# Performance work log

Measured on AMD Instinct MI355X. Metric: run time of the kernel, lower is better.

The kernel has to match this reference:

```python
import jax, jax.numpy as jnp
import numpy as np

H = 32          # total heads
K = 8           # active heads per token
D = 128         # head_dim = embed_dim // active_heads
E = 1024        # embed_dim
S = 1024        # seq_len
MAX_SEQ = 8192
BASE = 10000.0
SCALE = D ** -0.5
LB_W = 0.01
ENT_W = 0.01


def _rope(v, cos, sin):
    # v: (T, D); cos/sin: (T, D)
    v1, v2 = v[:, : D // 2], v[:, D // 2:]
    rot = jnp.concatenate([-v2, v1], axis=-1)
    return v * cos + rot * sin


def setup_inputs() -> dict:
    key = jax.random.key(0)
    ks = jax.random.split(key, 6)
    x = jax.random.normal(ks[0], (1, S, E), jnp.float32)
    Wq = jax.random.normal(ks[1], (E, H * D), jnp.float32) * 0.02
    Wk = jax.random.normal(ks[2], (E, H * D), jnp.float32) * 0.02
    Wv = jax.random.normal(ks[3], (E, H * D), jnp.float32) * 0.02
    Wr = jax.random.normal(ks[4], (E, H), jnp.float32) * 0.02
    Wo = jax.random.normal(ks[5], (K * D, E), jnp.float32) * 0.02
    head_counts = jnp.zeros((1, H), jnp.int32)
    return {"x": x, "Wq": Wq, "Wk": Wk, "Wv": Wv, "Wr": Wr, "Wo": Wo,
            "head_counts": head_counts}


def reference(x, Wq, Wk, Wv, Wr, Wo, head_counts):
    # ---- routing (eval mode: no gumbel noise) ----
    logits = x @ Wr                                   # (1, S, H)
    soft_probs = jax.nn.softmax(logits, axis=-1)
    top_logits, head_idx = jax.lax.top_k(logits, K)   # (1, S, K)
    head_w = jax.nn.softmax(top_logits, axis=-1)      # (1, S, K)

    # ---- aux loss ----
    primary = head_idx[..., 0]                        # (1, S)
    one_hot_p = jax.nn.one_hot(primary, H, dtype=jnp.float32)
    f = one_hot_p.mean(axis=1)                        # (1, H)
    p = soft_probs.mean(axis=1)                       # (1, H)
    balance = H * (f * p).sum(axis=-1).mean()
    entropy = -(soft_probs * jnp.log(soft_probs + 1e-8)).sum(axis=-1)
    entropy_loss = -entropy.mean()
    z_loss = (jax.nn.logsumexp(logits, axis=-1) ** 2).mean() * 0.01
    aux_loss = LB_W * balance + ENT_W * entropy_loss + z_loss

    # ---- projections + per-token gather of selected heads ----
    q_all = (x @ Wq).reshape(1, S, H, D)
    k_all = (x @ Wk).reshape(1, S, H, D)
    v_all = (x @ Wv).reshape(1, S, H, D)
    gidx = head_idx[..., None]                        # (1, S, K, 1)
    q = jnp.take_along_axis(q_all, gidx, axis=2)[0].reshape(S * K, D)
    k = jnp.take_along_axis(k_all, gidx, axis=2)[0].reshape(S * K, D)
    v = jnp.take_along_axis(v_all, gidx, axis=2)[0].reshape(S * K, D)

    heads_flat = head_idx[0].reshape(S * K)           # (T,)

    # rank of each dispatched token within its head (exclusive prefix count)
    oh = jax.nn.one_hot(heads_flat, H, dtype=jnp.int32)   # (T, H)
    excl = jnp.cumsum(oh, axis=0) - oh
    rank = jnp.take_along_axis(excl, heads_flat[:, None], axis=1)[:, 0]
    positions = rank + head_counts[0, heads_flat]
    positions = jnp.clip(positions, 0, MAX_SEQ - 1)

    # ---- per-head RoPE with per-head position counters ----
    inv_freq = 1.0 / (BASE ** (jnp.arange(0, D, 2, dtype=jnp.float32) / D))
    freqs = positions.astype(jnp.float32)[:, None] * inv_freq[None, :]
    emb = jnp.concatenate([freqs, freqs], axis=-1)    # (T, D)
    cos, sin = jnp.cos(emb), jnp.sin(emb)
    q = _rope(q, cos, sin)
    k = _rope(k, cos, sin)

    # ---- block-diagonal-causal attention (same head, earlier dispatch order) ----
    idx = jnp.arange(S * K)
    mask = (heads_flat[:, None] == heads_flat[None, :]) & (idx[None, :] <= idx[:, None])
    scores = (q @ k.T) * SCALE                        # (T, T)
    scores = jnp.where(mask, scores, jnp.float32(-1e30))
    attn = jax.nn.softmax(scores, axis=-1)
    out = attn @ v                                    # (T, D)

    # ---- combine with routing weights + output projection ----
    out = out.reshape(S, K, D) * head_w[0][..., None]
    out = out.reshape(S, K * D) @ Wo                  # (S, E)
    output = out[None]                                # (1, S, E)

    updated_counts = head_counts + oh.sum(axis=0)[None]
    return output, updated_counts, aux_loss
```

## Files before the change

### kernel.cpp

```cpp
#include <hip/hip_runtime.h>
#include <math.h>

#define S 1024
#define E 1024
#define H 32
#define KSEL 8
#define D 128
#define HD 4096
#define SK 8192
#define MAXL 1024
#define CAP 9216
#define ATTN_SCALE 0.08838834764831845f
#define SSTR 36
#define PSTR 40

#define NROUTER 256
#define NCONV 832

typedef _Float16 half8 __attribute__((ext_vector_type(8)));
typedef _Float16 half4 __attribute__((ext_vector_type(4)));
typedef float floatx4 __attribute__((ext_vector_type(4)));
typedef float floatx16 __attribute__((ext_vector_type(16)));
typedef float f4 __attribute__((ext_vector_type(4)));

#define GLOAD_LDS16(gsrc, ldst) \
    __builtin_amdgcn_global_load_lds( \
        (const __attribute__((address_space(1))) void*)(gsrc), \
        (__attribute__((address_space(3))) void*)(ldst), 16, 0, 0)

__global__ __launch_bounds__(256) void router_conv_kernel(
    const float* __restrict__ x, const float* __restrict__ Wr,
    int* __restrict__ head_idx, float* __restrict__ head_w,
    float* __restrict__ pbuf, float* __restrict__ entz,
    _Float16* __restrict__ xh,
    const float* __restrict__ Wq, const float* __restrict__ Wk,
    const float* __restrict__ Wv, const float* __restrict__ Wo,
    _Float16* __restrict__ Wqkt, _Float16* __restrict__ Wot)
{
    int bid = blockIdx.x, tid = threadIdx.x;
    if (bid >= NROUTER) {
        __shared__ _Float16 tl[128 * 128];
        int cb = bid - NROUTER;
        int z, rem;
        if (cb < 768) { z = cb >> 8; rem = cb & 255; }
        else          { z = 3;       rem = cb - 768; }
        const float* W = (z == 0) ? Wq : (z == 1) ? Wk : (z == 2) ? Wv : Wo;
        _Float16* T = (z < 3) ? (Wqkt + (size_t)z * HD * E) : Wot;
        int C = (z < 3) ? HD : 1024;
        int nc = C >> 7;
        int c0 = (rem % nc) * 128;
        int r0 = (rem / nc) * 128;
        #pragma unroll
        for (int p = 0; p < 16; ++p) {
            int idx = p * 256 + tid;
            int rr = idx >> 5, cg = (idx & 31) * 4;
            f4 v = *(const f4*)&W[(size_t)(r0 + rr) * C + c0 + cg];
            half4 o;
            o.x = (_Float16)v.x; o.y = (_Float16)v.y;
            o.z = (_Float16)v.z; o.w = (_Float16)v.w;
            int sc = cg ^ (((rr >> 3) & 7) << 2);
            *(half4*)&tl[rr * 128 + sc] = o;
        }
        __syncthreads();
        #pragma unroll
        for (int p = 0; p < 8; ++p) {
            int chunk = p * 256 + tid;
            int cc = chunk >> 4, ch = chunk & 15;
            int cidx = cc ^ ((ch & 7) << 2);
            half8 o;
            #pragma unroll
            for (int j = 0; j < 8; ++j)
                o[j] = tl[(ch * 8 + j) * 128 + cidx];
            *(half8*)&T[(size_t)(c0 + cc) * 1024 + r0 + ch * 8] = o;
        }
        return;
    }
    int s = bid * 4 + (tid >> 6);
    int lane = tid & 63;
    int h = lane & 31, half = lane >> 5;
    const float* xr = x + (size_t)s * E + half * 512;
    const float* wr = Wr + (size_t)(half * 512) * H + h;
    float a0 = 0.f, a1 = 0.f, a2 = 0.f, a3 = 0.f;
    #pragma unroll 4
    for (int e = 0; e < 512; e += 4) {
        a0 += xr[e]     * wr[e * H];
        a1 += xr[e + 1] * wr[(e + 1) * H];
        a2 += xr[e + 2] * wr[(e + 2) * H];
        a3 += xr[e + 3] * wr[(e + 3) * H];
    }
    float acc = (a0 + a1) + (a2 + a3);
    acc += __shfl_xor(acc, 32, 64);
    float logit = acc;
    float m = logit;
    #pragma unroll
    for (int off = 16; off; off >>= 1) m = fmaxf(m, __shfl_xor(m, off, 64));
    float ex = expf(logit - m);
    float Z = ex;
    #pragma unroll
    for (int off = 16; off; off >>= 1) Z += __shfl_xor(Z, off, 64);
    float p = ex / Z;
    float es = p * logf(p + 1e-8f);
    #pragma unroll
    for (int off = 16; off; off >>= 1) es += __shfl_xor(es, off, 64);
    float lse = m + logf(Z);
    float lv = logit;
    float tv[KSEL]; int ti[KSEL];
    #pragma unroll
    for (int j = 0; j < KSEL; ++j) {
        float bv = lv; int bi = h;
        #pragma unroll
        for (int off = 16; off; off >>= 1) {
            float ov = __shfl_xor(bv, off, 64);
            int oi = __shfl_xor(bi, off, 64);
            if (ov > bv || (ov == bv && oi < bi)) { bv = ov; bi = oi; }
        }
        tv[j] = bv; ti[j] = bi;
        if (h == bi) lv = -INFINITY;
    }
    float Z2 = 0.f;
    #pragma unroll
    for (int j = 0; j < KSEL; ++j) Z2 += expf(tv[j] - tv[0]);
    if (lane < 32) pbuf[s * 32 + lane] = p;
    if (lane == 0) {
        entz[s * 2]     = es;
        entz[s * 2 + 1] = lse * lse;
        #pragma unroll
        for (int j = 0; j < KSEL; ++j) {
            head_idx[s * KSEL + j] = ti[j];
            head_w[s * KSEL + j]   = expf(tv[j] - tv[0]) / Z2;
        }
    }
    const float* xrow = x + (size_t)s * E;
    _Float16* xhrow = xh + (size_t)s * E;
    #pragma unroll
    for (int t = 0; t < 4; ++t) {
        int e = t * 256 + lane * 4;
        f4 v = *(const f4*)&xrow[e];
        half4 o;
        o.x = (_Float16)v.x; o.y = (_Float16)v.y; o.z = (_Float16)v.z; o.w = (_Float16)v.w;
        *(half4*)&xhrow[e] = o;
    }
}

__global__ __launch_bounds__(256) void scan_aux_kernel(
    const int* __restrict__ head_idx, const int* __restrict__ head_counts,
    int* __restrict__ order, int* __restrict__ hlen, float* __restrict__ out_counts,
    const float* __restrict__ pbuf, const float* __restrict__ entz,
    float* __restrict__ out_aux)
{
    int bid = blockIdx.x, tid = threadIdx.x;
    if (bid == H) {
        int hh = tid & 31, grp = tid >> 5;
        __shared__ float red[256], red2[256];
        __shared__ float psum[32];
        __shared__ int hist[32];
        if (tid < 32) hist[tid] = 0;
        float ps = 0.f;
        for (int s = grp; s < S; s += 8) ps += pbuf[s * 32 + hh];
        red[tid] = ps;
        float es = 0.f, zs = 0.f;
        for (int s = tid; s < S; s += 256) { es += entz[s * 2]; zs += entz[s * 2 + 1]; }
        red2[tid] = es;
        __syncthreads();
        if (grp == 0) {
            float v = 0.f;
            #pragma unroll
            for (int j = 0; j < 8; ++j) v += red[j * 32 + hh];
            psum[hh] = v;
        }
        __syncthreads();
        red[tid] = zs;
        for (int s = tid; s < S; s += 256)
            atomicAdd(&hist[head_idx[s * KSEL]], 1);
        __syncthreads();
        for (int stp = 128; stp; stp >>= 1) {
            if (tid < stp) { red[tid] += red[tid + stp]; red2[tid] += red2[tid + stp]; }
            __syncthreads();
        }
        if (tid == 0) {
            float bal = 0.f;
            for (int j = 0; j < H; ++j)
                bal += ((float)hist[j] / (float)S) * (psum[j] / (float)S);
            bal *= (float)H;
            float ent_loss = red2[0] / (float)S;
            float z = red[0] / (float)S * 0.01f;
            out_aux[0] = 0.01f * bal + 0.01f * ent_loss + z;
        }
        return;
    }
    int h = bid;
    int wave = tid >> 6, lane = tid & 63;
    __shared__ int wtot[4][4];
    int base = 0;
    int hc = head_counts[h];
    int v0 = head_idx[tid],       v1 = head_idx[256 + tid];
    int v2 = head_idx[512 + tid], v3 = head_idx[768 + tid];
    unsigned long long lt = (1ull << lane) - 1ull;
    for (int c0 = 0; c0 < SK; c0 += 1024) {
        int n0 = 0, n1 = 0, n2 = 0, n3 = 0;
        if (c0 + 1024 < SK) {
            n0 = head_idx[c0 + 1024 + tid]; n1 = head_idx[c0 + 1280 + tid];
            n2 = head_idx[c0 + 1536 + tid]; n3 = head_idx[c0 + 1792 + tid];
        }
        bool p0 = (v0 == h), p1 = (v1 == h), p2 = (v2 == h), p3 = (v3 == h);
        unsigned long long m0 = __ballot(p0), m1 = __ballot(p1);
        unsigned long long m2 = __ballot(p2), m3 = __ballot(p3);
        int w0 = __popcll(m0 & lt), w1 = __popcll(m1 & lt);
        int w2 = __popcll(m2 & lt), w3 = __popcll(m3 & lt);
        if (lane == 0) {
            wtot[0][wave] = __popcll(m0); wtot[1][wave] = __popcll(m1);
            wtot[2][wave] = __popcll(m2); wtot[3][wave] = __popcll(m3);
        }
        __syncthreads();
        int pw[4], T[4];
        #pragma unroll
        for (int i = 0; i < 4; ++i) {
            int pre = 0, tot = 0;
            #pragma unroll
            for (int w = 0; w < 4; ++w) {
                int tv = wtot[i][w];
                if (w < wave) pre += tv;
                tot += tv;
            }
            pw[i] = pre; T[i] = tot;
        }
        if (p0) order[h * MAXL + base + pw[0] + w0] = c0 + tid;
        if (p1) order[h * MAXL + base + T[0] + pw[1] + w1] = c0 + 256 + tid;
        if (p2) order[h * MAXL + base + T[0] + T[1] + pw[2] + w2] = c0 + 512 + tid;
        if (p3) order[h * MAXL + base + T[0] + T[1] + T[2] + pw[3] + w3] = c0 + 768 + tid;
        base += T[0] + T[1] + T[2] + T[3];
        __syncthreads();
        v0 = n0; v1 = n1; v2 = n2; v3 = n3;
    }
    if (tid == 0) {
        hlen[h] = base;
        out_counts[h] = (float)(hc + base);
    }
}

__global__ __launch_bounds__(256) void qkv_mfma(
    const _Float16* __restrict__ xh, const _Float16* __restrict__ Wt,
    const int* __restrict__ order, const int* __restrict__ hlen,
    const int* __restrict__ head_counts,
    _Float16* __restrict__ qh, _Float16* __restrict__ kh, _Float16* __restrict__ vT)
{
    int xid = blockIdx.x;
    int qkv = xid >> 5, h = xid & 31;
    int rt = blockIdx.y;
    int len = hlen[h];
    int row0 = rt * 64;
    if (row0 >= len) return;
    int hb = 0;
    for (int i = 0; i < h; ++i) hb += (hlen[i] + 31) & ~31;
    int lenp = (len + 31) & ~31;
    int tid = threadIdx.x, wave = tid >> 6, lane = tid & 63;
    int wm = wave >> 1, wn = wave & 1;
    int l32 = lane & 31, g = lane >> 5;

    __shared__ _Float16 Bs[2][128 * 64];

    int arow_g = row0 + wm * 32 + l32;
    int tok = (arow_g < len) ? (order[h * MAXL + arow_g] >> 3) : 0;
    const _Float16* aptr = xh + (size_t)tok * E;

    const _Float16* Wb = Wt + (size_t)((qkv * H + h) * D) * E;

    auto stageB = [&](int buf, int k0) {
        #pragma unroll
        for (int it = 0; it < 4; ++it) {
            int f = it * 256 + tid;
            int row = f >> 3, c = f & 7;
            int sc = c ^ (row & 7);
            const _Float16* src = Wb + (size_t)row * E + k0 + sc * 8;
            GLOAD_LDS16(src, &Bs[buf][f * 8]);
        }
    };

    floatx16 acc[2] = {};
    half8 a_cur[4], a_nxt[4];
    #pragma unroll
    for (int ks = 0; ks < 4; ++ks)
        a_cur[ks] = *(const half8*)(aptr + ks * 16 + g * 8);

    auto compute = [&](int buf, half8* a) {
        #pragma unroll
        for (int ks = 0; ks < 4; ++ks) {
            int wchunk = ks * 2 + g;
            #pragma unroll
            for (int nf = 0; nf < 2; ++nf) {
                int brow = wn * 64 + nf * 32 + l32;
                half8 bf = *(const half8*)&Bs[buf][brow * 64 + (wchunk ^ (brow & 7)) * 8];
                acc[nf] = __builtin_amdgcn_mfma_f32_32x32x16_f16(a[ks], bf, acc[nf], 0, 0, 0);
            }
        }
    };

    stageB(0, 0);
    __syncthreads();
    int buf = 0;
    for (int k0 = 64; k0 < E; k0 += 64) {
        stageB(buf ^ 1, k0);
        #pragma unroll
        for (int ks = 0; ks < 4; ++ks)
            a_nxt[ks] = *(const half8*)(aptr + k0 + ks * 16 + g * 8);
        compute(buf, a_cur);
        __syncthreads();
        buf ^= 1;
        #pragma unroll
        for (int ks = 0; ks < 4; ++ks) a_cur[ks] = a_nxt[ks];
    }
    compute(buf, a_cur);

    if (qkv < 2) {
        _Float16* dst = (qkv == 0) ? qh : kh;
        float* scr = (float*)&Bs[0][0];
        __syncthreads();
        #pragma unroll
        for (int nf = 0; nf < 2; ++nf) {
            int col = wn * 64 + nf * 32 + l32;
            #pragma unroll
            for (int reg = 0; reg < 16; ++reg) {
                int rl = wm * 32 + (reg & 3) + 8 * (reg >> 2) + 4 * g;
                scr[rl * 128 + col] = acc[nf][reg];
            }
        }
        __syncthreads();
        int hc = head_counts[h];
        #pragma unroll
        for (int pass = 0; pass < 16; ++pass) {
            int idx = pass * 256 + tid;
            int r = idx >> 6, d2 = idx & 63;
            int slot = row0 + r;
            if (slot < len) {
                float v1 = scr[r * 128 + d2], v2 = scr[r * 128 + 64 + d2];
                int p = slot + hc;
                p = p < 0 ? 0 : (p > 8191 ? 8191 : p);
                float inv = exp2f((float)d2 * -0.20762050f);
                float ang = (float)p * inv;
                float cs = cosf(ang), sn = sinf(ang);
                _Float16* dp = dst + ((size_t)hb + slot) * D;
                dp[d2]      = (_Float16)(v1 * cs - v2 * sn);
                dp[d2 + 64] = (_Float16)(v2 * cs + v1 * sn);
            }
        }
    } else {
        #pragma unroll
        for (int nf = 0; nf < 2; ++nf) {
            int col = wn * 64 + nf * 32 + l32;
            #pragma unroll
            for (int q4 = 0; q4 < 4; ++q4) {
                int slot0 = row0 + wm * 32 + 8 * q4 + 4 * g;
                _Float16* vp = vT + (size_t)hb * D + (size_t)col * lenp + slot0;
                if (slot0 + 3 < len) {
                    half4 o;
                    o.x = (_Float16)acc[nf][q4 * 4 + 0];
                    o.y = (_Float16)acc[nf][q4 * 4 + 1];
                    o.z = (_Float16)acc[nf][q4 * 4 + 2];
                    o.w = (_Float16)acc[nf][q4 * 4 + 3];
                    *(half4*)vp = o;
                } else {
                    #pragma unroll
                    for (int r2 = 0; r2 < 4; ++r2)
                        if (slot0 + r2 < len) vp[r2] = (_Float16)acc[nf][q4 * 4 + r2];
                }
            }
        }
    }
}

__global__ __launch_bounds__(128) void attn_mfma(
    const _Float16* __restrict__ qh, const _Float16* __restrict__ kh,
    const _Float16* __restrict__ vT,
    const int* __restrict__ order, const int* __restrict__ hlen,
    const float* __restrict__ head_w, _Float16* __restrict__ ao)
{
    int h = blockIdx.x >> 5, qt = blockIdx.x & 31;
    int len = hlen[h];
    int row0 = qt * 32;
    if (row0 >= len) return;
    int hb = 0;
    for (int i = 0; i < h; ++i) hb += (hlen[i] + 31) & ~31;
    int lenp = (len + 31) & ~31;
    int tid = threadIdx.x;
    int w = tid >> 6, lane = tid & 63;
    int l32 = lane & 31, g = lane >> 5;
    int srow = lane >> 1, shalf = lane & 1;

    __shared__ float Sld[2][32 * SSTR];
    __shared__ _Float16 Pld[2][32 * PSTR];
    __shared__ float alphaLd[2][32];
    __shared__ float mlLd[32][4];
    __shared__ float facLd[32][3];
    __shared__ int flatLd[32];
    __shared__ float Obuf[32][128];

    if (tid < 32) {
        int r = row0 + tid;
        flatLd[tid] = (r < len) ? order[h * MAXL + r] : -1;
    }

    const _Float16* qrow = qh + ((size_t)hb + row0 + l32) * D;
    half8 qf[8];
    #pragma unroll
    for (int t = 0; t < 8; ++t) qf[t] = *(const half8*)(qrow + t * 16 + g * 8);

    floatx16 O[4] = {};
    float m_run = -INFINITY, l_run = 0.f;

    if (w <= qt) {
        half8 kf[8], kfn[8], vv[8];
        {
            const _Float16* krow = kh + ((size_t)hb + w * 32 + l32) * D;
            #pragma unroll
            for (int t = 0; t < 8; ++t) kf[t] = *(const half8*)(krow + t * 16 + g * 8);
        }
        for (int kt = w; kt <= qt; kt += 2) {
            int col0 = kt * 32;
            floatx16 Sc = {};
            #pragma unroll
            for (int t = 0; t < 8; ++t)
                Sc = __builtin_amdgcn_mfma_f32_32x32x16_f16(qf[t], kf[t], Sc, 0, 0, 0);
            #pragma unroll
            for (int nt = 0; nt < 4; ++nt) {
                const _Float16* vp = vT + (size_t)hb * D + (size_t)(nt * 32 + l32) * lenp + col0;
                vv[nt * 2]     = *(const half8*)(vp + g * 8);
                vv[nt * 2 + 1] = *(const half8*)(vp + 16 + g * 8);
            }
            if (kt + 2 <= qt) {
                const _Float16* krow = kh + ((size_t)hb + col0 + 64 + l32) * D;
                #pragma unroll
                for (int t = 0; t < 8; ++t) kfn[t] = *(const half8*)(krow + t * 16 + g * 8);
            }
            bool diag = (kt == qt);
            #pragma unroll
            for (int reg = 0; reg < 16; ++reg) {
                int row = (reg & 3) + 8 * (reg >> 2) + 4 * g;
                float s = Sc[reg] * ATTN_SCALE;
                if (diag && l32 > row) s = -1e30f;
                Sld[w][row * SSTR + l32] = s;
            }
            __builtin_amdgcn_wave_barrier();
            const float* sp = &Sld[w][srow * SSTR + shalf * 16];
            float va[16];
            *(f4*)(va)      = *(const f4*)(sp);
            *(f4*)(va + 4)  = *(const f4*)(sp + 4);
            *(f4*)(va + 8)  = *(const f4*)(sp + 8);
            *(f4*)(va + 12) = *(const f4*)(sp + 12);
            float mt_ = va[0];
            #pragma unroll
            for (int j = 1; j < 16; ++j) mt_ = fmaxf(mt_, va[j]);
            mt_ = fmaxf(mt_, __shfl_xor(mt_, 1, 64));
            float m_new = fmaxf(m_run, mt_);
            float alpha = __expf(m_run - m_new);
            float p[16], tsum = 0.f;
            #pragma unroll
            for (int j = 0; j < 16; ++j) { p[j] = __expf(va[j] - m_new); tsum += p[j]; }
            tsum += __shfl_xor(tsum, 1, 64);
            l_run = l_run * alpha + tsum;
            m_run = m_new;
            half8 ph0, ph1;
            #pragma unroll
            for (int j = 0; j < 8; ++j) { ph0[j] = (_Float16)p[j]; ph1[j] = (_Float16)p[j + 8]; }
            *(half8*)&Pld[w][srow * PSTR + shalf * 16]     = ph0;
            *(half8*)&Pld[w][srow * PSTR + shalf * 16 + 8] = ph1;
            if (shalf == 0) alphaLd[w][srow] = alpha;
            __builtin_amdgcn_wave_barrier();
            f4 al[4];
            #pragma unroll
            for (int qq = 0; qq < 4; ++qq) al[qq] = *(const f4*)&alphaLd[w][4 * g + 8 * qq];
            #pragma unroll
            for (int reg = 0; reg < 16; ++reg) {
                float av = al[reg >> 2][reg & 3];
                O[0][reg] *= av; O[1][reg] *= av; O[2][reg] *= av; O[3][reg] *= av;
            }
            half8 pf0 = *(const half8*)&Pld[w][l32 * PSTR + g * 8];
            half8 pf1 = *(const half8*)&Pld[w][l32 * PSTR + 16 + g * 8];
            #pragma unroll
            for (int nt = 0; nt < 4; ++nt) {
                O[nt] = __builtin_amdgcn_mfma_f32_32x32x16_f16(pf0, vv[nt * 2],     O[nt], 0, 0, 0);
                O[nt] = __builtin_amdgcn_mfma_f32_32x32x16_f16(pf1, vv[nt * 2 + 1], O[nt], 0, 0, 0);
            }
            __builtin_amdgcn_wave_barrier();
            #pragma unroll
            for (int t = 0; t < 8; ++t) kf[t] = kfn[t];
        }
    }
    if (shalf == 0) { mlLd[srow][w * 2] = m_run; mlLd[srow][w * 2 + 1] = l_run; }
    __syncthreads();
    if (tid < 32) {
        float m0 = mlLd[tid][0], l0 = mlLd[tid][1];
        float m1 = mlLd[tid][2], l1 = mlLd[tid][3];
        float ms = fmaxf(m0, m1);
        float f0 = __expf(m0 - ms), f1 = __expf(m1 - ms);
        float lt = f0 * l0 + f1 * l1;
        int flat = flatLd[tid];
        float hw = (flat >= 0) ? head_w[flat] : 0.f;
        facLd[tid][0] = f1;
        facLd[tid][1] = hw / lt;
        facLd[tid][2] = f0;
    }
    __syncthreads();
    if (w == 1) {
        #pragma unroll
        for (int nt = 0; nt < 4; ++nt) {
            int col = nt * 32 + l32;
            #pragma unroll
            for (int reg = 0; reg < 16; ++reg) {
                int row = (reg & 3) + 8 * (reg >> 2) + 4 * g;
                Obuf[row][col] = O[nt][reg] * facLd[row][0];
            }
        }
    }
    __syncthreads();
    if (w == 0) {
        #pragma unroll
        for (int nt = 0; nt < 4; ++nt) {
            int col = nt * 32 + l32;
            #pragma unroll
            for (int reg = 0; reg < 16; ++reg) {
                int row = (reg & 3) + 8 * (reg >> 2) + 4 * g;
                int flat = flatLd[row];
                if (flat >= 0) {
                    float val = (O[nt][reg] * facLd[row][2] + Obuf[row][col]) * facLd[row][1];
                    ao[(size_t)flat * D + col] = (_Float16)val;
                }
            }
        }
    }
}

__global__ __launch_bounds__(256) void out_mfma(
    const _Float16* __restrict__ A, const _Float16* __restrict__ Bt,
    float* __restrict__ C)
{
    int n0 = blockIdx.x * 64, m0 = blockIdx.y * 64;
    int tid = threadIdx.x, wave = tid >> 6, lane = tid & 63;
    int wm = wave >> 1, wn = wave & 1;
    int l32 = lane & 31, g = lane >> 5;

    __shared__ _Float16 Bs[2][64 * 64];

    const _Float16* aptr = A + (size_t)(m0 + wm * 32 + l32) * 1024;

    auto stageB = [&](int buf, int k0) {
        #pragma unroll
        for (int it = 0; it < 2; ++it) {
            int f = it * 256 + tid;
            int row = f >> 3, c = f & 7;
            int sc = c ^ (row & 7);
            GLOAD_LDS16(Bt + (size_t)(n0 + row) * 1024 + k0 + sc * 8, &Bs[buf][f * 8]);
        }
    };

    floatx16 acc = {};
    int brow = wn * 32 + l32;
    half8 a_cur[4], a_nxt[4];
    #pragma unroll
    for (int ks = 0; ks < 4; ++ks)
        a_cur[ks] = *(const half8*)(aptr + ks * 16 + g * 8);

    auto compute = [&](int buf, half8* a) {
        #pragma unroll
        for (int ks = 0; ks < 4; ++ks) {
            int wchunk = ks * 2 + g;
            half8 bf = *(const half8*)&Bs[buf][brow * 64 + (wchunk ^ (brow & 7)) * 8];
            acc = __builtin_amdgcn_mfma_f32_32x32x16_f16(a[ks], bf, acc, 0, 0, 0);
        }
    };

    stageB(0, 0);
    __syncthreads();
    int buf = 0;
    for (int k0 = 64; k0 < 1024; k0 += 64) {
        stageB(buf ^ 1, k0);
        #pragma unroll
        for (int ks = 0; ks < 4; ++ks)
            a_nxt[ks] = *(const half8*)(aptr + k0 + ks * 16 + g * 8);
        compute(buf, a_cur);
        __syncthreads();
        buf ^= 1;
        #pragma unroll
        for (int ks = 0; ks < 4; ++ks) a_cur[ks] = a_nxt[ks];
    }
    compute(buf, a_cur);

    int col = n0 + wn * 32 + l32;
    #pragma unroll
    for (int reg = 0; reg < 16; ++reg) {
        int row = m0 + wm * 32 + (reg & 3) + 8 * (reg >> 2) + 4 * g;
        C[(size_t)row * 1024 + col] = acc[reg];
    }
}

extern "C" void kernel_launch(void* const* d_in, const int* in_sizes, int n_in,
                              void* d_out, int out_size, void* d_ws, size_t ws_size,
                              hipStream_t stream)
{
    const float* x  = (const float*)d_in[0];
    const float* Wq = (const float*)d_in[1];
    const float* Wk = (const float*)d_in[2];
    const float* Wv = (const float*)d_in[3];
    const float* Wr = (const float*)d_in[4];
    const float* Wo = (const float*)d_in[5];
    const int* head_counts = (const int*)d_in[6];
    float* out = (float*)d_out;

    float* head_w = (float*)d_ws;
    float* pbuf   = head_w + SK;
    float* entz   = pbuf + S * 32;
    int* head_idx = (int*)(entz + S * 2);
    int* order    = head_idx + SK;
    int* hlen     = order + H * MAXL;
    _Float16* xh   = (_Float16*)(hlen + 64);
    _Float16* aoh  = xh + (size_t)S * E;
    _Float16* Wqkt = aoh + (size_t)SK * D;
    _Float16* Wot  = Wqkt + (size_t)3 * HD * E;
    _Float16* qh   = Wot + (size_t)1024 * 1024;
    _Float16* kh   = qh + (size_t)CAP * D;
    _Float16* vT   = kh + (size_t)CAP * D;

    router_conv_kernel<<<NROUTER + NCONV, 256, 0, stream>>>(
        x, Wr, head_idx, head_w, pbuf, entz, xh, Wq, Wk, Wv, Wo, Wqkt, Wot);
    scan_aux_kernel<<<33, 256, 0, stream>>>(head_idx, head_counts, order, hlen,
                                            out + (size_t)S * E, pbuf, entz,
                                            out + (size_t)S * E + H);
    qkv_mfma<<<dim3(96, 16), 256, 0, stream>>>(xh, Wqkt, order, hlen, head_counts,
                                               qh, kh, vT);
    attn_mfma<<<H * 32, 128, 0, stream>>>(qh, kh, vT, order, hlen, head_w, aoh);
    out_mfma<<<dim3(16, 16), 256, 0, stream>>>(aoh, Wot, out);
}
```

Before: 222.4 us.

## Fuse QKV projection and attention into persistent kernel with per-head readiness counters

Merges the QKV projection and attention kernels into one persistent kernel. Blocks pull work tickets from an atomic counter. Attention tiles for a head spin on a per-head counter until all of that head's QKV tiles are done, so attention on finished heads overlaps projection on others. It also precomputes a cos/sin RoPE table in the first kernel instead of calling sincos per element, and packs two 32-row query tiles per 256-thread block. The risks are spin-wait overhead, added atomic traffic, and a possible deadlock if ticket order and residency interact badly.

```diff
diff --git a/kernel.cpp b/kernel.cpp
--- a/kernel.cpp
+++ b/kernel.cpp
@@ -16,10 +16,13 @@
 
 #define NROUTER 256
 #define NCONV 832
+#define NTAB 512
+#define NQKV_T 1536
+#define NATTN_T 512
+#define NTICK (NQKV_T + NATTN_T)
 
 typedef _Float16 half8 __attribute__((ext_vector_type(8)));
 typedef _Float16 half4 __attribute__((ext_vector_type(4)));
-typedef float floatx4 __attribute__((ext_vector_type(4)));
 typedef float floatx16 __attribute__((ext_vector_type(16)));
 typedef float f4 __attribute__((ext_vector_type(4)));
 
@@ -35,9 +38,24 @@
     _Float16* __restrict__ xh,
     const float* __restrict__ Wq, const float* __restrict__ Wk,
     const float* __restrict__ Wv, const float* __restrict__ Wo,
-    _Float16* __restrict__ Wqkt, _Float16* __restrict__ Wot)
+    _Float16* __restrict__ Wqkt, _Float16* __restrict__ Wot,
+    float2* __restrict__ tab)
 {
     int bid = blockIdx.x, tid = threadIdx.x;
+    if (bid >= NROUTER + NCONV) {
+        int base = (bid - NROUTER - NCONV) * 1024;
+        #pragma unroll
+        for (int j = 0; j < 4; ++j) {
+            int idx = base + j * 256 + tid;
+            int p = idx >> 6, d2 = idx & 63;
+            float inv = exp2f((float)d2 * -0.20762050f);
+            float ang = (float)p * inv;
+            float sn, cs;
+            sincosf(ang, &sn, &cs);
+            tab[idx] = make_float2(cs, sn);
+        }
+        return;
+    }
     if (bid >= NROUTER) {
         __shared__ _Float16 tl[128 * 128];
         int cb = bid - NROUTER;
@@ -146,10 +164,11 @@
     const int* __restrict__ head_idx, const int* __restrict__ head_counts,
     int* __restrict__ order, int* __restrict__ hlen, float* __restrict__ out_counts,
     const float* __restrict__ pbuf, const float* __restrict__ entz,
-    float* __restrict__ out_aux)
+    float* __restrict__ out_aux, int* __restrict__ syncb)
 {
     int bid = blockIdx.x, tid = threadIdx.x;
     if (bid == H) {
+        if (tid < 40) syncb[tid] = 0;
         int hh = tid & 31, grp = tid >> 5;
         __shared__ float red[256], red2[256];
         __shared__ float psum[32];
@@ -238,31 +257,33 @@
     }
 }
 
-__global__ __launch_bounds__(256) void qkv_mfma(
-    const _Float16* __restrict__ xh, const _Float16* __restrict__ Wt,
+
+__device__ __forceinline__ void do_qkv_tile(
+    int id, const _Float16* __restrict__ xh, const _Float16* __restrict__ Wt,
     const int* __restrict__ order, const int* __restrict__ hlen,
-    const int* __restrict__ head_counts,
-    _Float16* __restrict__ qh, _Float16* __restrict__ kh, _Float16* __restrict__ vT)
+    const int* __restrict__ head_counts, const float2* __restrict__ tab,
+    _Float16* __restrict__ qh, _Float16* __restrict__ kh, _Float16* __restrict__ vT,
+    char* smem, int* syncb, int tid)
 {
-    int xid = blockIdx.x;
-    int qkv = xid >> 5, h = xid & 31;
-    int rt = blockIdx.y;
+    int h = id / 48;
+    int sub = id - h * 48;
+    int qkv = sub >> 4;
+    int rt = sub & 15;
     int len = hlen[h];
     int row0 = rt * 64;
     if (row0 >= len) return;
     int hb = 0;
     for (int i = 0; i < h; ++i) hb += (hlen[i] + 31) & ~31;
     int lenp = (len + 31) & ~31;
-    int tid = threadIdx.x, wave = tid >> 6, lane = tid & 63;
+    int wave = tid >> 6, lane = tid & 63;
     int wm = wave >> 1, wn = wave & 1;
     int l32 = lane & 31, g = lane >> 5;
 
-    __shared__ _Float16 Bs[2][128 * 64];
+    _Float16* Bs = (_Float16*)smem;
 
     int arow_g = row0 + wm * 32 + l32;
     int tok = (arow_g < len) ? (order[h * MAXL + arow_g] >> 3) : 0;
     const _Float16* aptr = xh + (size_t)tok * E;
-
     const _Float16* Wb = Wt + (size_t)((qkv * H + h) * D) * E;
 
     auto stageB = [&](int buf, int k0) {
@@ -272,7 +293,7 @@
             int row = f >> 3, c = f & 7;
             int sc = c ^ (row & 7);
             const _Float16* src = Wb + (size_t)row * E + k0 + sc * 8;
-            GLOAD_LDS16(src, &Bs[buf][f * 8]);
+            GLOAD_LDS16(src, &Bs[buf * 8192 + f * 8]);
         }
     };
 
@@ -289,7 +310,7 @@
             #pragma unroll
             for (int nf = 0; nf < 2; ++nf) {
                 int brow = wn * 64 + nf * 32 + l32;
-                half8 bf = *(const half8*)&Bs[buf][brow * 64 + (wchunk ^ (brow & 7)) * 8];
+                half8 bf = *(const half8*)&Bs[buf * 8192 + brow * 64 + (wchunk ^ (brow & 7)) * 8];
                 acc[nf] = __builtin_amdgcn_mfma_f32_32x32x16_f16(a[ks], bf, acc[nf], 0, 0, 0);
             }
         }
@@ -313,7 +334,7 @@
 
     if (qkv < 2) {
         _Float16* dst = (qkv == 0) ? qh : kh;
-        float* scr = (float*)&Bs[0][0];
+        float* scr = (float*)smem;
         __syncthreads();
         #pragma unroll
         for (int nf = 0; nf < 2; ++nf) {
@@ -335,12 +356,10 @@
                 float v1 = scr[r * 128 + d2], v2 = scr[r * 128 + 64 + d2];
                 int p = slot + hc;
                 p = p < 0 ? 0 : (p > 8191 ? 8191 : p);
-                float inv = exp2f((float)d2 * -0.20762050f);
-                float ang = (float)p * inv;
-                float cs = cosf(ang), sn = sinf(ang);
+                float2 tt = tab[p * 64 + d2];
                 _Float16* dp = dst + ((size_t)hb + slot) * D;
-                dp[d2]      = (_Float16)(v1 * cs - v2 * sn);
-                dp[d2 + 64] = (_Float16)(v2 * cs + v1 * sn);
+                dp[d2]      = (_Float16)(v1 * tt.x - v2 * tt.y);
+                dp[d2 + 64] = (_Float16)(v2 * tt.x + v1 * tt.y);
             }
         }
     } else {
@@ -366,60 +385,77 @@
             }
         }
     }
+    __syncthreads();
+    if (tid == 0)
+        __hip_atomic_fetch_add(&syncb[1 + h], 1, __ATOMIC_RELEASE, __HIP_MEMORY_SCOPE_AGENT);
 }
 
-__global__ __launch_bounds__(128) void attn_mfma(
-    const _Float16* __restrict__ qh, const _Float16* __restrict__ kh,
-    const _Float16* __restrict__ vT,
-    const int* __restrict__ order, const int* __restrict__ hlen,
-    const float* __restrict__ head_w, _Float16* __restrict__ ao)
+__device__ __forceinline__ void do_attn_pair(
+    int id2, const _Float16* __restrict__ qh, const _Float16* __restrict__ kh,
+    const _Float16* __restrict__ vT, const int* __restrict__ order,
+    const int* __restrict__ hlen, const float* __restrict__ head_w,
+    _Float16* __restrict__ ao, char* smem, int* syncb, int tid)
 {
-    int h = blockIdx.x >> 5, qt = blockIdx.x & 31;
+    int h = id2 >> 4, t = id2 & 15;
     int len = hlen[h];
+    if (t * 64 >= len) return;
+    int need = 3 * ((len + 63) >> 6);
+    if (tid == 0) {
+        while (__hip_atomic_load(&syncb[1 + h], __ATOMIC_ACQUIRE, __HIP_MEMORY_SCOPE_AGENT) < need)
+            __builtin_amdgcn_s_sleep(2);
+    }
+    __syncthreads();
+
+    int hh = tid >> 7;
+    int lt = tid & 127;
+    int wl = lt >> 6, lane = lt & 63;
+    int l32 = lane & 31, g = lane >> 5;
+    int srow = lane >> 1, shalf = lane & 1;
+
+    char* hb_ = smem + hh * 17536;
+    float* Sld = (float*)hb_;
+    _Float16* Pld = (_Float16*)(hb_ + 9216);
+    float* alphaLd = (float*)(hb_ + 14336);
+    float* Obuf = (float*)hb_;
+    float* mlLd = (float*)(hb_ + 16384);
+    float* facLd = (float*)(hb_ + 16896);
+    int* flatLd = (int*)(hb_ + 17408);
+
+    int qt = t * 2 + hh;
     int row0 = qt * 32;
-    if (row0 >= len) return;
+    bool alive = row0 < len;
+    int row0c = alive ? row0 : 0;
+
     int hb = 0;
     for (int i = 0; i < h; ++i) hb += (hlen[i] + 31) & ~31;
     int lenp = (len + 31) & ~31;
-    int tid = threadIdx.x;
-    int w = tid >> 6, lane = tid & 63;
-    int l32 = lane & 31, g = lane >> 5;
-    int srow = lane >> 1, shalf = lane & 1;
-
-    __shared__ float Sld[2][32 * SSTR];
-    __shared__ _Float16 Pld[2][32 * PSTR];
-    __shared__ float alphaLd[2][32];
-    __shared__ float mlLd[32][4];
-    __shared__ float facLd[32][3];
-    __shared__ int flatLd[32];
-    __shared__ float Obuf[32][128];
-
-    if (tid < 32) {
-        int r = row0 + tid;
-        flatLd[tid] = (r < len) ? order[h * MAXL + r] : -1;
-    }
-
-    const _Float16* qrow = qh + ((size_t)hb + row0 + l32) * D;
+
+    if (lt < 32) {
+        int r = row0 + lt;
+        flatLd[lt] = (alive && r < len) ? order[h * MAXL + r] : -1;
+    }
+
+    const _Float16* qrow = qh + ((size_t)hb + row0c + l32) * D;
     half8 qf[8];
     #pragma unroll
-    for (int t = 0; t < 8; ++t) qf[t] = *(const half8*)(qrow + t * 16 + g * 8);
+    for (int tt = 0; tt < 8; ++tt) qf[tt] = *(const half8*)(qrow + tt * 16 + g * 8);
 
     floatx16 O[4] = {};
     float m_run = -INFINITY, l_run = 0.f;
 
-    if (w <= qt) {
+    if (alive && wl <= qt) {
         half8 kf[8], kfn[8], vv[8];
         {
-            const _Float16* krow = kh + ((size_t)hb + w * 32 + l32) * D;
-            #pragma unroll
-            for (int t = 0; t < 8; ++t) kf[t] = *(const half8*)(krow + t * 16 + g * 8);
-        }
-        for (int kt = w; kt <= qt; kt += 2) {
+            const _Float16* krow = kh + ((size_t)hb + wl * 32 + l32) * D;
+            #pragma unroll
+            for (int tt = 0; tt < 8; ++tt) kf[tt] = *(const half8*)(krow + tt * 16 + g * 8);
+        }
+        for (int kt = wl; kt <= qt; kt += 2) {
             int col0 = kt * 32;
             floatx16 Sc = {};
             #pragma unroll
-            for (int t = 0; t < 8; ++t)
-                Sc = __builtin_amdgcn_mfma_f32_32x32x16_f16(qf[t], kf[t], Sc, 0, 0, 0);
+            for (int tt = 0; tt < 8; ++tt)
+                Sc = __builtin_amdgcn_mfma_f32_32x32x16_f16(qf[tt], kf[tt], Sc, 0, 0, 0);
             #pragma unroll
             for (int nt = 0; nt < 4; ++nt) {
                 const _Float16* vp = vT + (size_t)hb * D + (size_t)(nt * 32 + l32) * lenp + col0;
@@ -429,7 +465,7 @@
             if (kt + 2 <= qt) {
                 const _Float16* krow = kh + ((size_t)hb + col0 + 64 + l32) * D;
                 #pragma unroll
-                for (int t = 0; t < 8; ++t) kfn[t] = *(const half8*)(krow + t * 16 + g * 8);
+                for (int tt = 0; tt < 8; ++tt) kfn[tt] = *(const half8*)(krow + tt * 16 + g * 8);
             }
             bool diag = (kt == qt);
             #pragma unroll
@@ -437,10 +473,10 @@
                 int row = (reg & 3) + 8 * (reg >> 2) + 4 * g;
                 float s = Sc[reg] * ATTN_SCALE;
                 if (diag && l32 > row) s = -1e30f;
-                Sld[w][row * SSTR + l32] = s;
+                Sld[wl * (32 * SSTR) + row * SSTR + l32] = s;
             }
             __builtin_amdgcn_wave_barrier();
-            const float* sp = &Sld[w][srow * SSTR + shalf * 16];
+            const float* sp = &Sld[wl * (32 * SSTR) + srow * SSTR + shalf * 16];
             float va[16];
             *(f4*)(va)      = *(const f4*)(sp);
             *(f4*)(va + 4)  = *(const f4*)(sp + 4);
@@ -461,20 +497,20 @@
             half8 ph0, ph1;
             #pragma unroll
             for (int j = 0; j < 8; ++j) { ph0[j] = (_Float16)p[j]; ph1[j] = (_Float16)p[j + 8]; }
-            *(half8*)&Pld[w][srow * PSTR + shalf * 16]     = ph0;
-            *(half8*)&Pld[w][srow * PSTR + shalf * 16 + 8] = ph1;
-            if (shalf == 0) alphaLd[w][srow] = alpha;
+            *(half8*)&Pld[wl * (32 * PSTR) + srow * PSTR + shalf * 16]     = ph0;
+            *(half8*)&Pld[wl * (32 * PSTR) + srow * PSTR + shalf * 16 + 8] = ph1;
+            if (shalf == 0) alphaLd[wl * 32 + srow] = alpha;
             __builtin_amdgcn_wave_barrier();
             f4 al[4];
             #pragma unroll
-            for (int qq = 0; qq < 4; ++qq) al[qq] = *(const f4*)&alphaLd[w][4 * g + 8 * qq];
+            for (int qq = 0; qq < 4; ++qq) al[qq] = *(const f4*)&alphaLd[wl * 32 + 4 * g + 8 * qq];
             #pragma unroll
             for (int reg = 0; reg < 16; ++reg) {
                 float av = al[reg >> 2][reg & 3];
                 O[0][reg] *= av; O[1][reg] *= av; O[2][reg] *= av; O[3][reg] *= av;
             }
-            half8 pf0 = *(const half8*)&Pld[w][l32 * PSTR + g * 8];
-            half8 pf1 = *(const half8*)&Pld[w][l32 * PSTR + 16 + g * 8];
+            half8 pf0 = *(const half8*)&Pld[wl * (32 * PSTR) + l32 * PSTR + g * 8];
+            half8 pf1 = *(const half8*)&Pld[wl * (32 * PSTR) + l32 * PSTR + 16 + g * 8];
             #pragma unroll
             for (int nt = 0; nt < 4; ++nt) {
                 O[nt] = __builtin_amdgcn_mfma_f32_32x32x16_f16(pf0, vv[nt * 2],     O[nt], 0, 0, 0);
@@ -482,37 +518,37 @@
             }
             __builtin_amdgcn_wave_barrier();
             #pragma unroll
-            for (int t = 0; t < 8; ++t) kf[t] = kfn[t];
-        }
-    }
-    if (shalf == 0) { mlLd[srow][w * 2] = m_run; mlLd[srow][w * 2 + 1] = l_run; }
+            for (int tt = 0; tt < 8; ++tt) kf[tt] = kfn[tt];
+        }
+    }
+    if (shalf == 0) { mlLd[srow * 4 + wl * 2] = m_run; mlLd[srow * 4 + wl * 2 + 1] = l_run; }
     __syncthreads();
-    if (tid < 32) {
-        float m0 = mlLd[tid][0], l0 = mlLd[tid][1];
-        float m1 = mlLd[tid][2], l1 = mlLd[tid][3];
+    if (lt < 32) {
+        float m0 = mlLd[lt * 4 + 0], l0 = mlLd[lt * 4 + 1];
+        float m1 = mlLd[lt * 4 + 2], l1 = mlLd[lt * 4 + 3];
         float ms = fmaxf(m0, m1);
         float f0 = __expf(m0 - ms), f1 = __expf(m1 - ms);
-        float lt = f0 * l0 + f1 * l1;
-        int flat = flatLd[tid];
+        float ltn = f0 * l0 + f1 * l1;
+        int flat = flatLd[lt];
         float hw = (flat >= 0) ? head_w[flat] : 0.f;
-        facLd[tid][0] = f1;
-        facLd[tid][1] = hw / lt;
-        facLd[tid][2] = f0;
+        facLd[lt * 4 + 0] = f1;
+        facLd[lt * 4 + 1] = hw / ltn;
+        facLd[lt * 4 + 2] = f0;
     }
     __syncthreads();
-    if (w == 1) {
+    if (wl == 1) {
         #pragma unroll
         for (int nt = 0; nt < 4; ++nt) {
             int col = nt * 32 + l32;
             #pragma unroll
             for (int reg = 0; reg < 16; ++reg) {
                 int row = (reg & 3) + 8 * (reg >> 2) + 4 * g;
-                Obuf[row][col] = O[nt][reg] * facLd[row][0];
+                Obuf[row * 128 + col] = O[nt][reg] * facLd[row * 4 + 0];
             }
         }
     }
     __syncthreads();
-    if (w == 0) {
+    if (wl == 0) {
         #pragma unroll
         for (int nt = 0; nt < 4; ++nt) {
             int col = nt * 32 + l32;
@@ -521,11 +557,36 @@
                 int row = (reg & 3) + 8 * (reg >> 2) + 4 * g;
                 int flat = flatLd[row];
                 if (flat >= 0) {
-                    float val = (O[nt][reg] * facLd[row][2] + Obuf[row][col]) * facLd[row][1];
+                    float val = (O[nt][reg] * facLd[row * 4 + 2] + Obuf[row * 128 + col]) * facLd[row * 4 + 1];
                     ao[(size_t)flat * D + col] = (_Float16)val;
                 }
             }
         }
+    }
+}
+
+__global__ __launch_bounds__(256) void qkv_attn(
+    const _Float16* __restrict__ xh, const _Float16* __restrict__ Wt,
+    const int* __restrict__ order, const int* __restrict__ hlen,
+    const int* __restrict__ head_counts, const float2* __restrict__ tab,
+    _Float16* __restrict__ qh, _Float16* __restrict__ kh, _Float16* __restrict__ vT,
+    const float* __restrict__ head_w, _Float16* __restrict__ ao,
+    int* __restrict__ syncb)
+{
+    __shared__ __align__(16) char smem[35072];
+    __shared__ int sh_id;
+    int tid = threadIdx.x;
+    while (true) {
+        __syncthreads();
+        if (tid == 0)
+            sh_id = __hip_atomic_fetch_add(&syncb[0], 1, __ATOMIC_RELAXED, __HIP_MEMORY_SCOPE_AGENT);
+        __syncthreads();
+        int id = sh_id;
+        if (id >= NTICK) break;
+        if (id < NQKV_T)
+            do_qkv_tile(id, xh, Wt, order, hlen, head_counts, tab, qh, kh, vT, smem, syncb, tid);
+        else
+            do_attn_pair(id - NQKV_T, qh, kh, vT, order, hlen, head_w, ao, smem, syncb, tid);
     }
 }
 
@@ -618,14 +679,15 @@
     _Float16* qh   = Wot + (size_t)1024 * 1024;
     _Float16* kh   = qh + (size_t)CAP * D;
     _Float16* vT   = kh + (size_t)CAP * D;
-
-    router_conv_kernel<<<NROUTER + NCONV, 256, 0, stream>>>(
-        x, Wr, head_idx, head_w, pbuf, entz, xh, Wq, Wk, Wv, Wo, Wqkt, Wot);
+    float2* tab    = (float2*)(vT + (size_t)CAP * D);
+    int* syncb     = (int*)(tab + (size_t)8192 * 64);
+
+    router_conv_kernel<<<NROUTER + NCONV + NTAB, 256, 0, stream>>>(
+        x, Wr, head_idx, head_w, pbuf, entz, xh, Wq, Wk, Wv, Wo, Wqkt, Wot, tab);
     scan_aux_kernel<<<33, 256, 0, stream>>>(head_idx, head_counts, order, hlen,
                                             out + (size_t)S * E, pbuf, entz,
-                                            out + (size_t)S * E + H);
-    qkv_mfma<<<dim3(96, 16), 256, 0, stream>>>(xh, Wqkt, order, hlen, head_counts,
-                                               qh, kh, vT);
-    attn_mfma<<<H * 32, 128, 0, stream>>>(qh, kh, vT, order, hlen, head_w, aoh);
+                                            out + (size_t)S * E + H, syncb);
+    qkv_attn<<<1024, 256, 0, stream>>>(xh, Wqkt, order, hlen, head_counts, tab,
+                                       qh, kh, vT, head_w, aoh, syncb);
     out_mfma<<<dim3(16, 16), 256, 0, stream>>>(aoh, Wot, out);
 }
```

After: 277.0 us. 24.6% more time.

## Fuse fp32 Wq/Wk/Wv conversion into QKV gather-GEMM and precompute RoPE table

Applied to the files above, without the earlier changes.

Drops the separate pass that converted and transposed Wq/Wk/Wv to fp16 in the router kernel. The QKV kernel now reads fp32 weights directly and converts them into swizzled LDS, with one block per (qkv, head, column-half) covering up to 1024 gathered rows. A cos/sin table for every position is built in the first kernel and replaces per-element sincos in the RoPE epilogue. This removes a large intermediate write/read of fp16 weights, but cuts the QKV grid to 192 blocks and makes the kernel load weights with strided scalar reads.

```diff
diff --git a/kernel.cpp b/kernel.cpp
--- a/kernel.cpp
+++ b/kernel.cpp
@@ -15,11 +15,11 @@
 #define PSTR 40
 
 #define NROUTER 256
-#define NCONV 832
+#define NCONV 64
+#define NTAB 512
 
 typedef _Float16 half8 __attribute__((ext_vector_type(8)));
 typedef _Float16 half4 __attribute__((ext_vector_type(4)));
-typedef float floatx4 __attribute__((ext_vector_type(4)));
 typedef float floatx16 __attribute__((ext_vector_type(16)));
 typedef float f4 __attribute__((ext_vector_type(4)));
 
@@ -33,28 +33,33 @@
     int* __restrict__ head_idx, float* __restrict__ head_w,
     float* __restrict__ pbuf, float* __restrict__ entz,
     _Float16* __restrict__ xh,
-    const float* __restrict__ Wq, const float* __restrict__ Wk,
-    const float* __restrict__ Wv, const float* __restrict__ Wo,
-    _Float16* __restrict__ Wqkt, _Float16* __restrict__ Wot)
+    const float* __restrict__ Wo, _Float16* __restrict__ Wot,
+    float2* __restrict__ tab)
 {
     int bid = blockIdx.x, tid = threadIdx.x;
+    if (bid >= NROUTER + NCONV) {
+        int base = (bid - NROUTER - NCONV) * 1024;
+        #pragma unroll
+        for (int j = 0; j < 4; ++j) {
+            int idx = base + j * 256 + tid;
+            int p = idx >> 6, d2 = idx & 63;
+            float inv = exp2f((float)d2 * -0.20762050f);
+            float ang = (float)p * inv;
+            float sn, cs;
+            sincosf(ang, &sn, &cs);
+            tab[idx] = make_float2(cs, sn);
+        }
+        return;
+    }
     if (bid >= NROUTER) {
         __shared__ _Float16 tl[128 * 128];
         int cb = bid - NROUTER;
-        int z, rem;
-        if (cb < 768) { z = cb >> 8; rem = cb & 255; }
-        else          { z = 3;       rem = cb - 768; }
-        const float* W = (z == 0) ? Wq : (z == 1) ? Wk : (z == 2) ? Wv : Wo;
-        _Float16* T = (z < 3) ? (Wqkt + (size_t)z * HD * E) : Wot;
-        int C = (z < 3) ? HD : 1024;
-        int nc = C >> 7;
-        int c0 = (rem % nc) * 128;
-        int r0 = (rem / nc) * 128;
+        int c0 = (cb & 7) * 128, r0 = (cb >> 3) * 128;
         #pragma unroll
         for (int p = 0; p < 16; ++p) {
             int idx = p * 256 + tid;
             int rr = idx >> 5, cg = (idx & 31) * 4;
-            f4 v = *(const f4*)&W[(size_t)(r0 + rr) * C + c0 + cg];
+            f4 v = *(const f4*)&Wo[(size_t)(r0 + rr) * 1024 + c0 + cg];
             half4 o;
             o.x = (_Float16)v.x; o.y = (_Float16)v.y;
             o.z = (_Float16)v.z; o.w = (_Float16)v.w;
@@ -71,7 +76,7 @@
             #pragma unroll
             for (int j = 0; j < 8; ++j)
                 o[j] = tl[(ch * 8 + j) * 128 + cidx];
-            *(half8*)&T[(size_t)(c0 + cc) * 1024 + r0 + ch * 8] = o;
+            *(half8*)&Wot[(size_t)(c0 + cc) * 1024 + r0 + ch * 8] = o;
         }
         return;
     }
@@ -238,130 +243,152 @@
     }
 }
 
-__global__ __launch_bounds__(256) void qkv_mfma(
-    const _Float16* __restrict__ xh, const _Float16* __restrict__ Wt,
+__global__ __launch_bounds__(512) void qkv_direct(
+    const _Float16* __restrict__ xh,
+    const float* __restrict__ Wq, const float* __restrict__ Wk, const float* __restrict__ Wv,
     const int* __restrict__ order, const int* __restrict__ hlen,
-    const int* __restrict__ head_counts,
+    const int* __restrict__ head_counts, const float2* __restrict__ tab,
     _Float16* __restrict__ qh, _Float16* __restrict__ kh, _Float16* __restrict__ vT)
 {
-    int xid = blockIdx.x;
-    int qkv = xid >> 5, h = xid & 31;
-    int rt = blockIdx.y;
+    int bid = blockIdx.x;
+    int hs = bid & 1;
+    int h  = (bid >> 1) & 31;
+    int z  = bid >> 6;
+    const float* W = (z == 0) ? Wq : (z == 1) ? Wk : Wv;
+
     int len = hlen[h];
-    int row0 = rt * 64;
-    if (row0 >= len) return;
     int hb = 0;
     for (int i = 0; i < h; ++i) hb += (hlen[i] + 31) & ~31;
     int lenp = (len + 31) & ~31;
-    int tid = threadIdx.x, wave = tid >> 6, lane = tid & 63;
-    int wm = wave >> 1, wn = wave & 1;
+
+    int tid = threadIdx.x;
+    int wv = tid >> 6;
+    int lane = tid & 63;
     int l32 = lane & 31, g = lane >> 5;
 
-    __shared__ _Float16 Bs[2][128 * 64];
-
-    int arow_g = row0 + wm * 32 + l32;
-    int tok = (arow_g < len) ? (order[h * MAXL + arow_g] >> 3) : 0;
-    const _Float16* aptr = xh + (size_t)tok * E;
-
-    const _Float16* Wb = Wt + (size_t)((qkv * H + h) * D) * E;
-
-    auto stageB = [&](int buf, int k0) {
-        #pragma unroll
-        for (int it = 0; it < 4; ++it) {
-            int f = it * 256 + tid;
-            int row = f >> 3, c = f & 7;
-            int sc = c ^ (row & 7);
-            const _Float16* src = Wb + (size_t)row * E + k0 + sc * 8;
-            GLOAD_LDS16(src, &Bs[buf][f * 8]);
-        }
-    };
-
-    floatx16 acc[2] = {};
-    half8 a_cur[4], a_nxt[4];
-    #pragma unroll
-    for (int ks = 0; ks < 4; ++ks)
-        a_cur[ks] = *(const half8*)(aptr + ks * 16 + g * 8);
-
-    auto compute = [&](int buf, half8* a) {
-        #pragma unroll
-        for (int ks = 0; ks < 4; ++ks) {
-            int wchunk = ks * 2 + g;
-            #pragma unroll
-            for (int nf = 0; nf < 2; ++nf) {
-                int brow = wn * 64 + nf * 32 + l32;
-                half8 bf = *(const half8*)&Bs[buf][brow * 64 + (wchunk ^ (brow & 7)) * 8];
-                acc[nf] = __builtin_amdgcn_mfma_f32_32x32x16_f16(a[ks], bf, acc[nf], 0, 0, 0);
-            }
-        }
-    };
-
-    stageB(0, 0);
-    __syncthreads();
-    int buf = 0;
-    for (int k0 = 64; k0 < E; k0 += 64) {
-        stageB(buf ^ 1, k0);
-        #pragma unroll
-        for (int ks = 0; ks < 4; ++ks)
-            a_nxt[ks] = *(const half8*)(aptr + k0 + ks * 16 + g * 8);
-        compute(buf, a_cur);
-        __syncthreads();
-        buf ^= 1;
-        #pragma unroll
-        for (int ks = 0; ks < 4; ++ks) a_cur[ks] = a_nxt[ks];
-    }
-    compute(buf, a_cur);
-
-    if (qkv < 2) {
-        _Float16* dst = (qkv == 0) ? qh : kh;
-        float* scr = (float*)&Bs[0][0];
-        __syncthreads();
-        #pragma unroll
-        for (int nf = 0; nf < 2; ++nf) {
-            int col = wn * 64 + nf * 32 + l32;
-            #pragma unroll
-            for (int reg = 0; reg < 16; ++reg) {
-                int rl = wm * 32 + (reg & 3) + 8 * (reg >> 2) + 4 * g;
-                scr[rl * 128 + col] = acc[nf][reg];
-            }
-        }
-        __syncthreads();
+    __shared__ _Float16 Bsh[64 * 512];
+
+    int scol = tid & 63;
+    int pscol = ((scol >> 5) << 6) + hs * 32 + (scol & 31);
+    const float* wcol = W + (size_t)h * D + pscol;
+
+    int npass = (len > 512) ? 2 : 1;
+    int tok[2][2];
+    #pragma unroll
+    for (int p = 0; p < 2; ++p)
+        #pragma unroll
+        for (int rt = 0; rt < 2; ++rt) {
+            int r = p * 512 + wv * 64 + rt * 32 + l32;
+            tok[p][rt] = (r < len) ? (order[h * MAXL + r] >> 3) : 0;
+        }
+
+    floatx16 acc[2][2][2] = {};
+
+    for (int khf = 0; khf < 2; ++khf) {
+        int kbase = khf * 512;
+        if (khf) __syncthreads();
+        {
+            int eg = tid >> 6;
+            const float* wp = wcol + (size_t)(kbase + eg * 8) * HD;
+            for (int rnd = 0; rnd < 8; ++rnd) {
+                float v[8];
+                #pragma unroll
+                for (int j = 0; j < 8; ++j) v[j] = wp[(size_t)j * HD];
+                half8 o;
+                #pragma unroll
+                for (int j = 0; j < 8; ++j) o[j] = (_Float16)v[j];
+                int e0 = rnd * 64 + eg * 8;
+                *(half8*)&Bsh[scol * 512 + (e0 ^ ((scol & 7) << 3))] = o;
+                wp += (size_t)64 * HD;
+            }
+        }
+        __syncthreads();
+        #pragma unroll
+        for (int p = 0; p < 2; ++p) {
+            if (p < npass) {
+                const _Float16* ap0 = xh + (size_t)tok[p][0] * E + kbase + g * 8;
+                const _Float16* ap1 = xh + (size_t)tok[p][1] * E + kbase + g * 8;
+                #pragma unroll 2
+                for (int kb = 0; kb < 8; ++kb) {
+                    half8 A0[4], A1[4];
+                    #pragma unroll
+                    for (int kc = 0; kc < 4; ++kc) {
+                        A0[kc] = *(const half8*)(ap0 + kb * 64 + kc * 16);
+                        A1[kc] = *(const half8*)(ap1 + kb * 64 + kc * 16);
+                    }
+                    #pragma unroll
+                    for (int kc = 0; kc < 4; ++kc) {
+                        int kk = kb * 64 + kc * 16 + g * 8;
+                        int kkx = kk ^ ((l32 & 7) << 3);
+                        half8 b0 = *(const half8*)&Bsh[l32 * 512 + kkx];
+                        half8 b1 = *(const half8*)&Bsh[(32 + l32) * 512 + kkx];
+                        acc[p][0][0] = __builtin_amdgcn_mfma_f32_32x32x16_f16(A0[kc], b0, acc[p][0][0], 0, 0, 0);
+                        acc[p][0][1] = __builtin_amdgcn_mfma_f32_32x32x16_f16(A0[kc], b1, acc[p][0][1], 0, 0, 0);
+                        acc[p][1][0] = __builtin_amdgcn_mfma_f32_32x32x16_f16(A1[kc], b0, acc[p][1][0], 0, 0, 0);
+                        acc[p][1][1] = __builtin_amdgcn_mfma_f32_32x32x16_f16(A1[kc], b1, acc[p][1][1], 0, 0, 0);
+                    }
+                }
+            }
+        }
+    }
+
+    if (z < 2) {
+        _Float16* dst = (z == 0) ? qh : kh;
         int hc = head_counts[h];
-        #pragma unroll
-        for (int pass = 0; pass < 16; ++pass) {
-            int idx = pass * 256 + tid;
-            int r = idx >> 6, d2 = idx & 63;
-            int slot = row0 + r;
-            if (slot < len) {
-                float v1 = scr[r * 128 + d2], v2 = scr[r * 128 + 64 + d2];
-                int p = slot + hc;
-                p = p < 0 ? 0 : (p > 8191 ? 8191 : p);
-                float inv = exp2f((float)d2 * -0.20762050f);
-                float ang = (float)p * inv;
-                float cs = cosf(ang), sn = sinf(ang);
-                _Float16* dp = dst + ((size_t)hb + slot) * D;
-                dp[d2]      = (_Float16)(v1 * cs - v2 * sn);
-                dp[d2 + 64] = (_Float16)(v2 * cs + v1 * sn);
+        int d2 = hs * 32 + l32;
+        #pragma unroll
+        for (int p = 0; p < 2; ++p) {
+            if (p < npass) {
+                #pragma unroll
+                for (int rt = 0; rt < 2; ++rt) {
+                    int base = p * 512 + wv * 64 + rt * 32;
+                    #pragma unroll
+                    for (int reg = 0; reg < 16; ++reg) {
+                        int slot = base + (reg & 3) + 8 * (reg >> 2) + 4 * g;
+                        if (slot < len) {
+                            int pos = slot + hc;
+                            pos = pos < 0 ? 0 : (pos > 8191 ? 8191 : pos);
+                            float2 tt = tab[pos * 64 + d2];
+                            float v1 = acc[p][rt][0][reg], v2 = acc[p][rt][1][reg];
+                            _Float16* dp = dst + ((size_t)hb + slot) * D;
+                            dp[d2]      = (_Float16)(v1 * tt.x - v2 * tt.y);
+                            dp[d2 + 64] = (_Float16)(v2 * tt.x + v1 * tt.y);
+                        }
+                    }
+                }
             }
         }
     } else {
         #pragma unroll
-        for (int nf = 0; nf < 2; ++nf) {
-            int col = wn * 64 + nf * 32 + l32;
-            #pragma unroll
-            for (int q4 = 0; q4 < 4; ++q4) {
-                int slot0 = row0 + wm * 32 + 8 * q4 + 4 * g;
-                _Float16* vp = vT + (size_t)hb * D + (size_t)col * lenp + slot0;
-                if (slot0 + 3 < len) {
-                    half4 o;
-                    o.x = (_Float16)acc[nf][q4 * 4 + 0];
-                    o.y = (_Float16)acc[nf][q4 * 4 + 1];
-                    o.z = (_Float16)acc[nf][q4 * 4 + 2];
-                    o.w = (_Float16)acc[nf][q4 * 4 + 3];
-                    *(half4*)vp = o;
-                } else {
+        for (int p = 0; p < 2; ++p) {
+            if (p < npass) {
+                #pragma unroll
+                for (int rt = 0; rt < 2; ++rt) {
+                    int base = p * 512 + wv * 64 + rt * 32;
                     #pragma unroll
-                    for (int r2 = 0; r2 < 4; ++r2)
-                        if (slot0 + r2 < len) vp[r2] = (_Float16)acc[nf][q4 * 4 + r2];
+                    for (int nf = 0; nf < 2; ++nf) {
+                        int pcol = nf * 64 + hs * 32 + l32;
+                        _Float16* vp0 = vT + (size_t)hb * D + (size_t)pcol * lenp;
+                        #pragma unroll
+                        for (int q4 = 0; q4 < 4; ++q4) {
+                            int slot0 = base + 8 * q4 + 4 * g;
+                            if (slot0 + 3 < len) {
+                                half4 o;
+                                o.x = (_Float16)acc[p][rt][nf][q4 * 4 + 0];
+                                o.y = (_Float16)acc[p][rt][nf][q4 * 4 + 1];
+                                o.z = (_Float16)acc[p][rt][nf][q4 * 4 + 2];
+                                o.w = (_Float16)acc[p][rt][nf][q4 * 4 + 3];
+                                *(half4*)(vp0 + slot0) = o;
+                            } else {
+                                #pragma unroll
+                                for (int r2 = 0; r2 < 4; ++r2) {
+                                    int sl = slot0 + r2;
+                                    if (sl < len) vp0[sl] = (_Float16)acc[p][rt][nf][q4 * 4 + r2];
+                                    else if (sl < lenp) vp0[sl] = (_Float16)0.f;
+                                }
+                            }
+                        }
+                    }
                 }
             }
         }
@@ -613,19 +640,19 @@
     int* hlen     = order + H * MAXL;
     _Float16* xh   = (_Float16*)(hlen + 64);
     _Float16* aoh  = xh + (size_t)S * E;
-    _Float16* Wqkt = aoh + (size_t)SK * D;
-    _Float16* Wot  = Wqkt + (size_t)3 * HD * E;
+    _Float16* Wot  = aoh + (size_t)SK * D;
     _Float16* qh   = Wot + (size_t)1024 * 1024;
     _Float16* kh   = qh + (size_t)CAP * D;
     _Float16* vT   = kh + (size_t)CAP * D;
-
-    router_conv_kernel<<<NROUTER + NCONV, 256, 0, stream>>>(
-        x, Wr, head_idx, head_w, pbuf, entz, xh, Wq, Wk, Wv, Wo, Wqkt, Wot);
+    float2* tab    = (float2*)(vT + (size_t)CAP * D);
+
+    router_conv_kernel<<<NROUTER + NCONV + NTAB, 256, 0, stream>>>(
+        x, Wr, head_idx, head_w, pbuf, entz, xh, Wo, Wot, tab);
     scan_aux_kernel<<<33, 256, 0, stream>>>(head_idx, head_counts, order, hlen,
                                             out + (size_t)S * E, pbuf, entz,
                                             out + (size_t)S * E + H);
-    qkv_mfma<<<dim3(96, 16), 256, 0, stream>>>(xh, Wqkt, order, hlen, head_counts,
-                                               qh, kh, vT);
+    qkv_direct<<<192, 512, 0, stream>>>(xh, Wq, Wk, Wv, order, hlen, head_counts, tab,
+                                        qh, kh, vT);
     attn_mfma<<<H * 32, 128, 0, stream>>>(qh, kh, vT, order, hlen, head_w, aoh);
     out_mfma<<<dim3(16, 16), 256, 0, stream>>>(aoh, Wot, out);
 }
```

Result: no change. 222.1 us (-0.1%).
